# Kernel tuning notes

Hardware: AMD Instinct MI355X
Metric: run time of the kernel (lower is better)

Reference implementation:

```python
import jax, jax.numpy as jnp
import numpy as np

L, E, TOP_K = 3, 8, 2
B, N, D, DS = 256, 1024, 512, 128

def setup_inputs() -> dict:
    key = jax.random.key(0)
    ks = jax.random.split(key, 10)
    s = 0.05  # weight init scale
    return {
        "token": jax.random.normal(ks[0], (B, 1, D), jnp.float32),
        "node_emb": jax.random.normal(ks[1], (B, N, D), jnp.float32),
        "states": jnp.zeros((L, E, B, DS), jnp.float32),
        "Wg": jax.random.normal(ks[2], (L, D, E), jnp.float32) * s,
        "bg": jnp.zeros((L, E), jnp.float32),
        "A": jax.random.normal(ks[3], (L, E, DS), jnp.float32),
        "Bin": jax.random.normal(ks[4], (L, E, D, DS), jnp.float32) * s,
        "Cout": jax.random.normal(ks[5], (L, E, DS, D), jnp.float32) * s,
        "Dsk": jax.random.normal(ks[6], (L, E, D), jnp.float32) * s,
        "Wq": jax.random.normal(ks[7], (D, D), jnp.float32) * s,
        "bq": jnp.zeros((D,), jnp.float32),
    }

def reference(token, node_emb, states, Wg, bg, A, Bin, Cout, Dsk, Wq, bq):
    # token: (B,1,D) -> h: (B,D)
    h = token[:, 0, :]
    lb_loss = jnp.float32(0.0)
    new_states = []
    for l in range(L):
        # --- MoE router: top-k softmax gating ---
        probs = jax.nn.softmax(h @ Wg[l] + bg[l])              # (B,E)
        topv, topi = jax.lax.top_k(probs, TOP_K)               # (B,k)
        gates_k = topv / jnp.sum(topv, axis=-1, keepdims=True)  # renormalized
        oh = jax.nn.one_hot(topi, E, dtype=probs.dtype)        # (B,k,E)
        gate_full = jnp.einsum('bk,bke->be', gates_k, oh)      # (B,E)
        sel = jnp.sum(oh, axis=1) > 0                          # (B,E) bool
        # --- state-space experts (computed densely for all experts) ---
        s = states[l]                                          # (E,B,DS)
        decay = jax.nn.sigmoid(A[l])[:, None, :]               # (E,1,DS)
        s_new = decay * s + jnp.einsum('bd,eds->ebs', h, Bin[l])   # (E,B,DS)
        y = jnp.einsum('ebs,esd->ebd', s_new, Cout[l]) + h[None] * Dsk[l][:, None, :]
        out = jnp.einsum('be,ebd->bd', gate_full, y)           # weighted combine
        # only routed experts advance their state
        keep = sel.T[:, :, None]                               # (E,B,1)
        new_states.append(jnp.where(keep, s_new, s))
        # load-balance loss: E * sum_e mean(probs_e) * mean(frac routed to e)
        lb_loss = lb_loss + E * jnp.sum(jnp.mean(probs, axis=0) * jnp.mean(sel.astype(probs.dtype), axis=0))
        h = h + out                                            # residual
    # --- query projection + logits over nodes ---
    q = h @ Wq + bq                                            # (B,D)
    logits = jnp.einsum('bd,bnd->bn', q, node_emb) / jnp.sqrt(jnp.float32(D))
    return logits, jnp.stack(new_states), lb_loss
```

## Files before the change

### kernel.cpp

```cpp
#include <hip/hip_runtime.h>
#include <math.h>

#define LNUM 3
#define ENUM 8
#define TOPK 2
#define BSZ 256
#define NSZ 1024
#define DSZ 512
#define SSZ 128

typedef float f32x4 __attribute__((ext_vector_type(4)));

__global__ __launch_bounds__(1024, 2) void fused_kernel(
    const float* __restrict__ token,
    const float* __restrict__ states,
    const float* __restrict__ Wg,
    const float* __restrict__ bg,
    const float* __restrict__ A,
    const float* __restrict__ Bin,
    const float* __restrict__ Cout,
    const float* __restrict__ Dsk,
    const float* __restrict__ Wq,
    const float* __restrict__ bq,
    float* __restrict__ out_states,
    float* __restrict__ acc,
    float* __restrict__ q_out)
{
    const int b = blockIdx.x;
    const int t = threadIdx.x;
    const int wave = t >> 6;
    const int lane = t & 63;
    const int ehalf = t >> 9;

    __shared__ float h_s[DSZ];
    __shared__ float snew_s[TOPK][SSZ];
    __shared__ float logit_s[ENUM];
    __shared__ f32x4 part4[1024];
    float* part = (float*)part4;

    if (t < DSZ) h_s[t] = token[b * DSZ + t];

    for (int l = 0; l < LNUM; ++l) {
        const float* Wg_l  = Wg  + (size_t)l * DSZ * ENUM;
        const float* bg_l  = bg  + (size_t)l * ENUM;
        const float* A_l   = A   + (size_t)l * ENUM * SSZ;
        const float* Bin_l = Bin + (size_t)l * ENUM * DSZ * SSZ;
        const float* Cou_l = Cout+ (size_t)l * ENUM * SSZ * DSZ;
        const float* Dsk_l = Dsk + (size_t)l * ENUM * DSZ;
        const float* st_l  = states     + (size_t)l * ENUM * BSZ * SSZ;
        float*       os_l  = out_states + (size_t)l * ENUM * BSZ * SSZ;

        __syncthreads();
        part4[t] = ((const f32x4*)Wg_l)[t];
        __syncthreads();

        if (wave < ENUM) {
            float p = 0.f;
            #pragma unroll
            for (int i = 0; i < 8; ++i) {
                const int d = lane + i * 64;
                p = fmaf(h_s[d], part[d * ENUM + wave], p);
            }
            for (int off = 32; off; off >>= 1) p += __shfl_down(p, off, 64);
            if (lane == 0) logit_s[wave] = p + bg_l[wave];
        }
        __syncthreads();

        float probs[ENUM];
        float mx = logit_s[0];
        for (int e = 1; e < ENUM; ++e) mx = fmaxf(mx, logit_s[e]);
        float ssum = 0.f;
        for (int e = 0; e < ENUM; ++e) { probs[e] = expf(logit_s[e] - mx); ssum += probs[e]; }
        const float sinv = 1.f / ssum;
        for (int e = 0; e < ENUM; ++e) probs[e] *= sinv;

        int i0 = 0;
        for (int e = 1; e < ENUM; ++e) if (probs[e] > probs[i0]) i0 = e;
        int i1 = -1;
        for (int e = 0; e < ENUM; ++e) {
            if (e == i0) continue;
            if (i1 < 0 || probs[e] > probs[i1]) i1 = e;
        }
        float g0 = probs[i0], g1 = probs[i1];
        const float ginv = 1.f / (g0 + g1);
        g0 *= ginv; g1 *= ginv;

        if (t < ENUM) {
            atomicAdd(&acc[(l * 2 + 0) * ENUM + t], probs[t]);
            atomicAdd(&acc[(l * 2 + 1) * ENUM + t], (t == i0 || t == i1) ? 1.0f : 0.0f);
        }
        const int esel = ehalf ? i1 : i0;

        {
            const int rem   = t & 511;
            const int c     = rem >> 5;
            const int squad = rem & 31;
            const float* Bp = Bin_l + (size_t)esel * DSZ * SSZ;
            const int d0 = c * 32;
            f32x4 acc4 = {0.f, 0.f, 0.f, 0.f};
            #pragma unroll
            for (int d = 0; d < 32; ++d)
                acc4 += *(const f32x4*)(Bp + (size_t)(d0 + d) * SSZ + squad * 4) * h_s[d0 + d];
            part4[(ehalf * 16 + c) * 32 + squad] = acc4;
        }
        __syncthreads();

        if (t < TOPK * SSZ) {
            const int k = t >> 7, s = t & 127;
            const int e = k ? i1 : i0;
            float sum = 0.f;
            #pragma unroll
            for (int c = 0; c < 16; ++c) sum += part[(k * 16 + c) * 128 + s];
            const float a = A_l[e * SSZ + s];
            const float decay = 1.f / (1.f + expf(-a));
            snew_s[k][s] = decay * st_l[((size_t)e * BSZ + b) * SSZ + s] + sum;
        }
        __syncthreads();

        {
            const int e = t >> 7, s = t & 127;
            float v;
            if (e == i0)      v = snew_s[0][s];
            else if (e == i1) v = snew_s[1][s];
            else              v = st_l[((size_t)e * BSZ + b) * SSZ + s];
            os_l[((size_t)e * BSZ + b) * SSZ + s] = v;
        }

        {
            const int rem   = t & 511;
            const int chunk = rem >> 7;
            const int dquad = rem & 127;
            const float* Cp = Cou_l + (size_t)esel * SSZ * DSZ;
            const float* sp = snew_s[ehalf];
            const int s0 = chunk * 32;
            f32x4 acc4 = {0.f, 0.f, 0.f, 0.f};
            #pragma unroll
            for (int s = 0; s < 32; ++s)
                acc4 += *(const f32x4*)(Cp + (size_t)(s0 + s) * DSZ + dquad * 4) * sp[s0 + s];
            part4[(ehalf * 4 + chunk) * 128 + dquad] = acc4;
        }
        __syncthreads();

        if (t < DSZ) {
            const float hd = h_s[t];
            float y0 = hd * Dsk_l[i0 * DSZ + t];
            float y1 = hd * Dsk_l[i1 * DSZ + t];
            #pragma unroll
            for (int c = 0; c < 4; ++c) {
                y0 += part[c * 512 + t];
                y1 += part[(4 + c) * 512 + t];
            }
            h_s[t] = hd + g0 * y0 + g1 * y1;
        }
    }

    __syncthreads();
    {
        const int chunk = t >> 7;
        const int dquad = t & 127;
        const int dd0 = chunk * 64;
        f32x4 acc4 = {0.f, 0.f, 0.f, 0.f};
        #pragma unroll 8
        for (int i = 0; i < 64; ++i)
            acc4 += *(const f32x4*)(Wq + (size_t)(dd0 + i) * DSZ + dquad * 4) * h_s[dd0 + i];
        part4[chunk * 128 + dquad] = acc4;
    }
    __syncthreads();
    if (t < DSZ) {
        float qv = bq[t];
        #pragma unroll
        for (int c = 0; c < 8; ++c) qv += part[c * 512 + t];
        q_out[b * DSZ + t] = qv;
    }
}

__global__ __launch_bounds__(256) void logits_kernel(
    const float* __restrict__ q, const float* __restrict__ node_emb,
    float* __restrict__ logits,
    const float* __restrict__ acc, float* __restrict__ loss_out)
{
    const int b = blockIdx.y;
    const int wave = threadIdx.x >> 6;
    const int lane = threadIdx.x & 63;

    if (blockIdx.x == 0 && blockIdx.y == 0 && threadIdx.x == 0) {
        float lb = 0.f;
        for (int l = 0; l < LNUM; ++l)
            for (int e = 0; e < ENUM; ++e) {
                const float mp = acc[(l * 2 + 0) * ENUM + e] * (1.0f / BSZ);
                const float ms = acc[(l * 2 + 1) * ENUM + e] * (1.0f / BSZ);
                lb += (float)ENUM * mp * ms;
            }
        loss_out[0] = lb;
    }

    const f32x4* q4 = (const f32x4*)(q + b * DSZ);
    const f32x4 q0 = q4[lane];
    const f32x4 q1 = q4[lane + 64];
    const float scale = 0.04419417382415922f;

    const int n0 = blockIdx.x * 128 + wave * 32;
    #pragma unroll 2
    for (int i = 0; i < 32; ++i) {
        const int n = n0 + i;
        const f32x4* r = (const f32x4*)(node_emb + ((size_t)b * NSZ + n) * DSZ);
        const f32x4 a0 = __builtin_nontemporal_load(&r[lane]);
        const f32x4 a1 = __builtin_nontemporal_load(&r[lane + 64]);
        float dot = a0.x * q0.x + a0.y * q0.y + a0.z * q0.z + a0.w * q0.w
                  + a1.x * q1.x + a1.y * q1.y + a1.z * q1.z + a1.w * q1.w;
        for (int off = 32; off; off >>= 1) dot += __shfl_down(dot, off, 64);
        if (lane == 0) logits[b * NSZ + n] = dot * scale;
    }
}

extern "C" void kernel_launch(void* const* d_in, const int* in_sizes, int n_in,
                              void* d_out, int out_size, void* d_ws, size_t ws_size,
                              hipStream_t stream) {
    const float* token    = (const float*)d_in[0];
    const float* node_emb = (const float*)d_in[1];
    const float* states   = (const float*)d_in[2];
    const float* Wg       = (const float*)d_in[3];
    const float* bg       = (const float*)d_in[4];
    const float* A        = (const float*)d_in[5];
    const float* Bin      = (const float*)d_in[6];
    const float* Cout     = (const float*)d_in[7];
    const float* Dsk      = (const float*)d_in[8];
    const float* Wq       = (const float*)d_in[9];
    const float* bq       = (const float*)d_in[10];

    float* out_logits = (float*)d_out;
    float* out_states = out_logits + (size_t)BSZ * NSZ;
    float* out_loss   = out_states + (size_t)LNUM * ENUM * BSZ * SSZ;

    float* ws_q   = (float*)d_ws;
    float* ws_acc = ws_q + (size_t)BSZ * DSZ;

    (void)hipMemsetAsync(ws_acc, 0, sizeof(float) * LNUM * 2 * ENUM, stream);

    fused_kernel<<<BSZ, 1024, 0, stream>>>(
        token, states, Wg, bg, A, Bin, Cout, Dsk, Wq, bq,
        out_states, ws_acc, ws_q);

    dim3 lg(NSZ / 128, BSZ);
    logits_kernel<<<lg, 256, 0, stream>>>(ws_q, node_emb, out_logits, ws_acc, out_loss);
}
```

Before: 172.5 us.

## Replace per-token kernels with single cooperative kernel using batched tiled GEMMs

Replaces the per-token fused kernel and the separate logits kernel with one cooperative grid kernel. Each layer runs as batched tiled GEMMs over all tokens: h·Bin is computed densely for all experts, then the state update, then a gated (B x E*DS)·Cout GEMM, with grid.sync between phases. The weights are read once per tile instead of once per token. The router is computed in separate blocks, and the load-balance loss is reduced without atomics or a memset. In exchange it computes all experts densely (up to 4x the FLOPs of top-2), adds several grid-wide barriers, and leaves most blocks idle in many phases.

```diff
diff --git a/kernel.cpp b/kernel.cpp
--- a/kernel.cpp
+++ b/kernel.cpp
@@ -1,215 +1,252 @@
 #include <hip/hip_runtime.h>
+#include <hip/hip_cooperative_groups.h>
 #include <math.h>
+
+namespace cg = cooperative_groups;
 
 #define LNUM 3
 #define ENUM 8
-#define TOPK 2
 #define BSZ 256
 #define NSZ 1024
 #define DSZ 512
 #define SSZ 128
 
 typedef float f32x4 __attribute__((ext_vector_type(4)));
-
-__global__ __launch_bounds__(1024, 2) void fused_kernel(
-    const float* __restrict__ token,
-    const float* __restrict__ states,
-    const float* __restrict__ Wg,
-    const float* __restrict__ bg,
-    const float* __restrict__ A,
-    const float* __restrict__ Bin,
-    const float* __restrict__ Cout,
-    const float* __restrict__ Dsk,
-    const float* __restrict__ Wq,
+typedef float f32x2 __attribute__((ext_vector_type(2)));
+
+__device__ __forceinline__ f32x2 gemm_tile(
+    float* __restrict__ sm, const float* __restrict__ Ap, int lda,
+    const float* __restrict__ Bp, int ldb, int K, int t)
+{
+    float* As = sm;
+    float* Bs = sm + 2112;
+    const int m  = t >> 5, np = t & 31;
+    const int ar = t >> 5, ak = (t & 31) * 2;
+    const int br = t >> 4, bq4 = (t & 15) * 4;
+    f32x2 acc = {0.f, 0.f};
+    for (int ks = 0; ks < K; ks += 64) {
+        __syncthreads();
+        *(f32x2*)&As[ar * 66 + ak] = *(const f32x2*)(Ap + (size_t)ar * lda + ks + ak);
+        *(f32x4*)&Bs[br * 64 + bq4] = *(const f32x4*)(Bp + (size_t)(ks + br) * ldb + bq4);
+        __syncthreads();
+        #pragma unroll
+        for (int k = 0; k < 64; ++k) {
+            const float a = As[m * 66 + k];
+            const f32x2 b2 = *(const f32x2*)&Bs[k * 64 + np * 2];
+            acc.x = fmaf(a, b2.x, acc.x);
+            acc.y = fmaf(a, b2.y, acc.y);
+        }
+    }
+    return acc;
+}
+
+__global__ __launch_bounds__(1024, 1) void coop_kernel(
+    const float* __restrict__ token, const float* __restrict__ node_emb,
+    const float* __restrict__ states, const float* __restrict__ Wg,
+    const float* __restrict__ bg, const float* __restrict__ A,
+    const float* __restrict__ Bin, const float* __restrict__ Cout,
+    const float* __restrict__ Dsk, const float* __restrict__ Wq,
     const float* __restrict__ bq,
-    float* __restrict__ out_states,
-    float* __restrict__ acc,
-    float* __restrict__ q_out)
+    float* __restrict__ out_logits, float* __restrict__ out_states,
+    float* __restrict__ out_loss,
+    float* __restrict__ hbuf, float* __restrict__ g1raw,
+    float* __restrict__ sng, float* __restrict__ gates,
+    float* __restrict__ accp, float* __restrict__ qbuf)
 {
-    const int b = blockIdx.x;
+    cg::grid_group grid = cg::this_grid();
+    const int bid = blockIdx.x;
     const int t = threadIdx.x;
-    const int wave = t >> 6;
-    const int lane = t & 63;
-    const int ehalf = t >> 9;
-
-    __shared__ float h_s[DSZ];
-    __shared__ float snew_s[TOPK][SSZ];
-    __shared__ float logit_s[ENUM];
-    __shared__ f32x4 part4[1024];
-    float* part = (float*)part4;
-
-    if (t < DSZ) h_s[t] = token[b * DSZ + t];
+    __shared__ __align__(16) float sm[10240];
 
     for (int l = 0; l < LNUM; ++l) {
-        const float* Wg_l  = Wg  + (size_t)l * DSZ * ENUM;
-        const float* bg_l  = bg  + (size_t)l * ENUM;
-        const float* A_l   = A   + (size_t)l * ENUM * SSZ;
+        const float* hsrc  = (l == 0) ? token : hbuf;
+        const float* Wg_l  = Wg + (size_t)l * DSZ * ENUM;
+        const float* bg_l  = bg + l * ENUM;
+        const float* A_l   = A + (size_t)l * ENUM * SSZ;
         const float* Bin_l = Bin + (size_t)l * ENUM * DSZ * SSZ;
-        const float* Cou_l = Cout+ (size_t)l * ENUM * SSZ * DSZ;
+        const float* Cou_l = Cout + (size_t)l * ENUM * SSZ * DSZ;
         const float* Dsk_l = Dsk + (size_t)l * ENUM * DSZ;
-        const float* st_l  = states     + (size_t)l * ENUM * BSZ * SSZ;
-        float*       os_l  = out_states + (size_t)l * ENUM * BSZ * SSZ;
-
+        const float* st_l  = states + (size_t)l * ENUM * BSZ * SSZ;
+        float* os_l        = out_states + (size_t)l * ENUM * BSZ * SSZ;
+
+        if (bid < 128) {
+            const int mt = bid >> 4, nt = bid & 15;
+            const int m0 = mt * 32, n0 = nt * 64;
+            const f32x2 acc = gemm_tile(sm, hsrc + (size_t)m0 * DSZ, DSZ,
+                                        Bin_l + (size_t)(nt >> 1) * DSZ * SSZ + (nt & 1) * 64,
+                                        SSZ, DSZ, t);
+            const int m = t >> 5, np = t & 31;
+            *(f32x2*)(g1raw + (size_t)(m0 + m) * 1024 + n0 + np * 2) = acc;
+        } else if (bid < 160) {
+            const int b0 = (bid - 128) * 8;
+            float* wg_s = sm;
+            float* h_s  = sm + 4096;
+            float* lgp  = sm + 8192;
+            float* lg   = sm + 9216;
+            float* ps   = sm + 9280;
+            float* sl   = sm + 9344;
+            ((f32x4*)wg_s)[t] = ((const f32x4*)Wg_l)[t];
+            ((f32x4*)h_s)[t]  = ((const f32x4*)(hsrc + (size_t)b0 * DSZ))[t];
+            __syncthreads();
+            {
+                const int tok = t >> 7, e = (t >> 4) & 7, kq = t & 15;
+                float p = 0.f;
+                #pragma unroll
+                for (int j = 0; j < 32; ++j) {
+                    const int d = kq + j * 16;
+                    p = fmaf(h_s[tok * DSZ + d], wg_s[d * ENUM + e], p);
+                }
+                lgp[t] = p;
+            }
+            __syncthreads();
+            if (t < 64) {
+                const int tok = t >> 3, e = t & 7;
+                float s = bg_l[e];
+                #pragma unroll
+                for (int kq = 0; kq < 16; ++kq) s += lgp[tok * 128 + e * 16 + kq];
+                lg[tok * 8 + e] = s;
+            }
+            __syncthreads();
+            if (t < 8) {
+                float probs[ENUM];
+                float mx = lg[t * 8];
+                for (int e = 1; e < ENUM; ++e) mx = fmaxf(mx, lg[t * 8 + e]);
+                float ss = 0.f;
+                for (int e = 0; e < ENUM; ++e) { probs[e] = expf(lg[t * 8 + e] - mx); ss += probs[e]; }
+                const float sinv = 1.f / ss;
+                for (int e = 0; e < ENUM; ++e) probs[e] *= sinv;
+                int i0 = 0;
+                for (int e = 1; e < ENUM; ++e) if (probs[e] > probs[i0]) i0 = e;
+                int i1 = -1;
+                for (int e = 0; e < ENUM; ++e) {
+                    if (e == i0) continue;
+                    if (i1 < 0 || probs[e] > probs[i1]) i1 = e;
+                }
+                const float gs = 1.f / (probs[i0] + probs[i1]);
+                for (int e = 0; e < ENUM; ++e) {
+                    const int selv = (e == i0 || e == i1) ? 1 : 0;
+                    gates[(b0 + t) * ENUM + e] = selv ? probs[e] * gs : 0.f;
+                    ps[t * 8 + e] = probs[e];
+                    sl[t * 8 + e] = (float)selv;
+                }
+            }
+            __syncthreads();
+            if (t < 16) {
+                const int e = t & 7;
+                float s = 0.f;
+                if (t < 8) {
+                    for (int tok = 0; tok < 8; ++tok) s += ps[tok * 8 + e];
+                    accp[((l * 32) + (bid - 128)) * 16 + e] = s;
+                } else {
+                    for (int tok = 0; tok < 8; ++tok) s += sl[tok * 8 + e];
+                    accp[((l * 32) + (bid - 128)) * 16 + 8 + e] = s;
+                }
+            }
+        }
+        grid.sync();
+
+        if (bid < 64) {
+            const int gid = bid * 1024 + t;
+            const int b = gid >> 8, nq = gid & 255;
+            const int e = nq >> 5, sq = (nq & 31) * 4;
+            const f32x4 g1q = *(const f32x4*)(g1raw + (size_t)b * 1024 + nq * 4);
+            const f32x4 stq = *(const f32x4*)(st_l + (size_t)e * BSZ * SSZ + b * SSZ + sq);
+            const f32x4 aq  = *(const f32x4*)(A_l + e * SSZ + sq);
+            f32x4 dec;
+            dec.x = 1.f / (1.f + expf(-aq.x));
+            dec.y = 1.f / (1.f + expf(-aq.y));
+            dec.z = 1.f / (1.f + expf(-aq.z));
+            dec.w = 1.f / (1.f + expf(-aq.w));
+            const f32x4 snew = dec * stq + g1q;
+            const float g = gates[b * ENUM + e];
+            *(f32x4*)(os_l + (size_t)e * BSZ * SSZ + b * SSZ + sq) = (g > 0.f) ? snew : stq;
+            *(f32x4*)(sng + (size_t)b * 1024 + nq * 4) = snew * g;
+        }
+        grid.sync();
+
+        if (bid < 64) {
+            const int mt = bid >> 3, nt = bid & 7;
+            const int m0 = mt * 32, n0 = nt * 64;
+            const f32x2 acc = gemm_tile(sm, sng + (size_t)m0 * 1024, 1024,
+                                        Cou_l + n0, DSZ, 1024, t);
+            const int m = t >> 5, np = t & 31;
+            const int b = m0 + m, d = n0 + np * 2;
+            float w0 = 0.f, w1 = 0.f;
+            #pragma unroll
+            for (int e = 0; e < ENUM; ++e) {
+                const float g = gates[b * ENUM + e];
+                w0 = fmaf(g, Dsk_l[e * DSZ + d], w0);
+                w1 = fmaf(g, Dsk_l[e * DSZ + d + 1], w1);
+            }
+            const f32x2 hold = *(const f32x2*)(hsrc + (size_t)b * DSZ + d);
+            f32x2 hn;
+            hn.x = hold.x + acc.x + hold.x * w0;
+            hn.y = hold.y + acc.y + hold.y * w1;
+            *(f32x2*)(hbuf + (size_t)b * DSZ + d) = hn;
+        }
+        grid.sync();
+    }
+
+    if (bid < 64) {
+        const int mt = bid >> 3, nt = bid & 7;
+        const int m0 = mt * 32, n0 = nt * 64;
+        const f32x2 acc = gemm_tile(sm, hbuf + (size_t)m0 * DSZ, DSZ,
+                                    Wq + n0, DSZ, DSZ, t);
+        const int m = t >> 5, np = t & 31;
+        const int d = n0 + np * 2;
+        f32x2 qv;
+        qv.x = acc.x + bq[d];
+        qv.y = acc.y + bq[d + 1];
+        *(f32x2*)(qbuf + (size_t)(m0 + m) * DSZ + d) = qv;
+    } else if (bid == 64) {
+        float* red = sm;
+        if (t < 24) {
+            const int l = t >> 3, e = t & 7;
+            float mp = 0.f, ms = 0.f;
+            for (int gb = 0; gb < 32; ++gb) {
+                mp += accp[(l * 32 + gb) * 16 + e];
+                ms += accp[(l * 32 + gb) * 16 + 8 + e];
+            }
+            red[t] = (float)ENUM * (mp * (1.f / BSZ)) * (ms * (1.f / BSZ));
+        }
         __syncthreads();
-        part4[t] = ((const f32x4*)Wg_l)[t];
-        __syncthreads();
-
-        if (wave < ENUM) {
-            float p = 0.f;
+        if (t == 0) {
+            float lb = 0.f;
+            for (int i = 0; i < 24; ++i) lb += red[i];
+            out_loss[0] = lb;
+        }
+    }
+    grid.sync();
+
+    {
+        const int b = bid;
+        const int wave = t >> 6, lane = t & 63;
+        const f32x4* q4 = (const f32x4*)(qbuf + (size_t)b * DSZ);
+        const f32x4 q0 = q4[lane];
+        const f32x4 q1 = q4[lane + 64];
+        const float scale = 0.04419417382415922f;
+        const int n0 = wave * 64;
+        for (int i = 0; i < 64; i += 2) {
+            const f32x4* r0 = (const f32x4*)(node_emb + ((size_t)b * NSZ + n0 + i) * DSZ);
+            const f32x4* r1 = (const f32x4*)(node_emb + ((size_t)b * NSZ + n0 + i + 1) * DSZ);
+            const f32x4 a0 = __builtin_nontemporal_load(r0 + lane);
+            const f32x4 a1 = __builtin_nontemporal_load(r0 + lane + 64);
+            const f32x4 c0 = __builtin_nontemporal_load(r1 + lane);
+            const f32x4 c1 = __builtin_nontemporal_load(r1 + lane + 64);
+            float d0 = a0.x*q0.x + a0.y*q0.y + a0.z*q0.z + a0.w*q0.w
+                     + a1.x*q1.x + a1.y*q1.y + a1.z*q1.z + a1.w*q1.w;
+            float d1 = c0.x*q0.x + c0.y*q0.y + c0.z*q0.z + c0.w*q0.w
+                     + c1.x*q1.x + c1.y*q1.y + c1.z*q1.z + c1.w*q1.w;
             #pragma unroll
-            for (int i = 0; i < 8; ++i) {
-                const int d = lane + i * 64;
-                p = fmaf(h_s[d], part[d * ENUM + wave], p);
-            }
-            for (int off = 32; off; off >>= 1) p += __shfl_down(p, off, 64);
-            if (lane == 0) logit_s[wave] = p + bg_l[wave];
-        }
-        __syncthreads();
-
-        float probs[ENUM];
-        float mx = logit_s[0];
-        for (int e = 1; e < ENUM; ++e) mx = fmaxf(mx, logit_s[e]);
-        float ssum = 0.f;
-        for (int e = 0; e < ENUM; ++e) { probs[e] = expf(logit_s[e] - mx); ssum += probs[e]; }
-        const float sinv = 1.f / ssum;
-        for (int e = 0; e < ENUM; ++e) probs[e] *= sinv;
-
-        int i0 = 0;
-        for (int e = 1; e < ENUM; ++e) if (probs[e] > probs[i0]) i0 = e;
-        int i1 = -1;
-        for (int e = 0; e < ENUM; ++e) {
-            if (e == i0) continue;
-            if (i1 < 0 || probs[e] > probs[i1]) i1 = e;
-        }
-        float g0 = probs[i0], g1 = probs[i1];
-        const float ginv = 1.f / (g0 + g1);
-        g0 *= ginv; g1 *= ginv;
-
-        if (t < ENUM) {
-            atomicAdd(&acc[(l * 2 + 0) * ENUM + t], probs[t]);
-            atomicAdd(&acc[(l * 2 + 1) * ENUM + t], (t == i0 || t == i1) ? 1.0f : 0.0f);
-        }
-        const int esel = ehalf ? i1 : i0;
-
-        {
-            const int rem   = t & 511;
-            const int c     = rem >> 5;
-            const int squad = rem & 31;
-            const float* Bp = Bin_l + (size_t)esel * DSZ * SSZ;
-            const int d0 = c * 32;
-            f32x4 acc4 = {0.f, 0.f, 0.f, 0.f};
-            #pragma unroll
-            for (int d = 0; d < 32; ++d)
-                acc4 += *(const f32x4*)(Bp + (size_t)(d0 + d) * SSZ + squad * 4) * h_s[d0 + d];
-            part4[(ehalf * 16 + c) * 32 + squad] = acc4;
-        }
-        __syncthreads();
-
-        if (t < TOPK * SSZ) {
-            const int k = t >> 7, s = t & 127;
-            const int e = k ? i1 : i0;
-            float sum = 0.f;
-            #pragma unroll
-            for (int c = 0; c < 16; ++c) sum += part[(k * 16 + c) * 128 + s];
-            const float a = A_l[e * SSZ + s];
-            const float decay = 1.f / (1.f + expf(-a));
-            snew_s[k][s] = decay * st_l[((size_t)e * BSZ + b) * SSZ + s] + sum;
-        }
-        __syncthreads();
-
-        {
-            const int e = t >> 7, s = t & 127;
-            float v;
-            if (e == i0)      v = snew_s[0][s];
-            else if (e == i1) v = snew_s[1][s];
-            else              v = st_l[((size_t)e * BSZ + b) * SSZ + s];
-            os_l[((size_t)e * BSZ + b) * SSZ + s] = v;
-        }
-
-        {
-            const int rem   = t & 511;
-            const int chunk = rem >> 7;
-            const int dquad = rem & 127;
-            const float* Cp = Cou_l + (size_t)esel * SSZ * DSZ;
-            const float* sp = snew_s[ehalf];
-            const int s0 = chunk * 32;
-            f32x4 acc4 = {0.f, 0.f, 0.f, 0.f};
-            #pragma unroll
-            for (int s = 0; s < 32; ++s)
-                acc4 += *(const f32x4*)(Cp + (size_t)(s0 + s) * DSZ + dquad * 4) * sp[s0 + s];
-            part4[(ehalf * 4 + chunk) * 128 + dquad] = acc4;
-        }
-        __syncthreads();
-
-        if (t < DSZ) {
-            const float hd = h_s[t];
-            float y0 = hd * Dsk_l[i0 * DSZ + t];
-            float y1 = hd * Dsk_l[i1 * DSZ + t];
-            #pragma unroll
-            for (int c = 0; c < 4; ++c) {
-                y0 += part[c * 512 + t];
-                y1 += part[(4 + c) * 512 + t];
-            }
-            h_s[t] = hd + g0 * y0 + g1 * y1;
-        }
-    }
-
-    __syncthreads();
-    {
-        const int chunk = t >> 7;
-        const int dquad = t & 127;
-        const int dd0 = chunk * 64;
-        f32x4 acc4 = {0.f, 0.f, 0.f, 0.f};
-        #pragma unroll 8
-        for (int i = 0; i < 64; ++i)
-            acc4 += *(const f32x4*)(Wq + (size_t)(dd0 + i) * DSZ + dquad * 4) * h_s[dd0 + i];
-        part4[chunk * 128 + dquad] = acc4;
-    }
-    __syncthreads();
-    if (t < DSZ) {
-        float qv = bq[t];
-        #pragma unroll
-        for (int c = 0; c < 8; ++c) qv += part[c * 512 + t];
-        q_out[b * DSZ + t] = qv;
-    }
-}
-
-__global__ __launch_bounds__(256) void logits_kernel(
-    const float* __restrict__ q, const float* __restrict__ node_emb,
-    float* __restrict__ logits,
-    const float* __restrict__ acc, float* __restrict__ loss_out)
-{
-    const int b = blockIdx.y;
-    const int wave = threadIdx.x >> 6;
-    const int lane = threadIdx.x & 63;
-
-    if (blockIdx.x == 0 && blockIdx.y == 0 && threadIdx.x == 0) {
-        float lb = 0.f;
-        for (int l = 0; l < LNUM; ++l)
-            for (int e = 0; e < ENUM; ++e) {
-                const float mp = acc[(l * 2 + 0) * ENUM + e] * (1.0f / BSZ);
-                const float ms = acc[(l * 2 + 1) * ENUM + e] * (1.0f / BSZ);
-                lb += (float)ENUM * mp * ms;
-            }
-        loss_out[0] = lb;
-    }
-
-    const f32x4* q4 = (const f32x4*)(q + b * DSZ);
-    const f32x4 q0 = q4[lane];
-    const f32x4 q1 = q4[lane + 64];
-    const float scale = 0.04419417382415922f;
-
-    const int n0 = blockIdx.x * 128 + wave * 32;
-    #pragma unroll 2
-    for (int i = 0; i < 32; ++i) {
-        const int n = n0 + i;
-        const f32x4* r = (const f32x4*)(node_emb + ((size_t)b * NSZ + n) * DSZ);
-        const f32x4 a0 = __builtin_nontemporal_load(&r[lane]);
-        const f32x4 a1 = __builtin_nontemporal_load(&r[lane + 64]);
-        float dot = a0.x * q0.x + a0.y * q0.y + a0.z * q0.z + a0.w * q0.w
-                  + a1.x * q1.x + a1.y * q1.y + a1.z * q1.z + a1.w * q1.w;
-        for (int off = 32; off; off >>= 1) dot += __shfl_down(dot, off, 64);
-        if (lane == 0) logits[b * NSZ + n] = dot * scale;
+            for (int off = 32; off; off >>= 1) {
+                d0 += __shfl_down(d0, off, 64);
+                d1 += __shfl_down(d1, off, 64);
+            }
+            if (lane == 0) {
+                out_logits[b * NSZ + n0 + i]     = d0 * scale;
+                out_logits[b * NSZ + n0 + i + 1] = d1 * scale;
+            }
+        }
     }
 }
 
@@ -232,15 +269,21 @@
     float* out_states = out_logits + (size_t)BSZ * NSZ;
     float* out_loss   = out_states + (size_t)LNUM * ENUM * BSZ * SSZ;
 
-    float* ws_q   = (float*)d_ws;
-    float* ws_acc = ws_q + (size_t)BSZ * DSZ;
-
-    (void)hipMemsetAsync(ws_acc, 0, sizeof(float) * LNUM * 2 * ENUM, stream);
-
-    fused_kernel<<<BSZ, 1024, 0, stream>>>(
-        token, states, Wg, bg, A, Bin, Cout, Dsk, Wq, bq,
-        out_states, ws_acc, ws_q);
-
-    dim3 lg(NSZ / 128, BSZ);
-    logits_kernel<<<lg, 256, 0, stream>>>(ws_q, node_emb, out_logits, ws_acc, out_loss);
+    float* hbuf  = (float*)d_ws;
+    float* g1raw = hbuf + 131072;
+    float* sng   = g1raw + 262144;
+    float* qbuf  = sng + 262144;
+    float* gates = qbuf + 131072;
+    float* accp  = gates + 2048;
+
+    void* args[] = {
+        (void*)&token, (void*)&node_emb, (void*)&states, (void*)&Wg, (void*)&bg,
+        (void*)&A, (void*)&Bin, (void*)&Cout, (void*)&Dsk, (void*)&Wq, (void*)&bq,
+        (void*)&out_logits, (void*)&out_states, (void*)&out_loss,
+        (void*)&hbuf, (void*)&g1raw, (void*)&sng, (void*)&gates,
+        (void*)&accp, (void*)&qbuf
+    };
+
+    (void)hipLaunchCooperativeKernel((const void*)coop_kernel,
+                                     dim3(256), dim3(1024), args, 0, stream);
 }
```

New measurement: 645.7 us. 274% more time.
